# Kernel optimization log

Measured on AMD Instinct MI355X. Metric: run time of the kernel, lower is better.

## Reference

```python
import jax, jax.numpy as jnp
import numpy as np


def setup_inputs() -> dict:
    key = jax.random.key(0)
    B, T, UNITS = 8, 4096, 1024
    # per-timestep features: [x, y, z_0..z_{units-1}]
    inputs = jax.random.normal(key, (B, T, UNITS + 2), dtype=jnp.float32)
    return {"inputs": inputs}


def reference(inputs) -> jnp.ndarray:
    # Faithful translation of CLSProcess wrapped in an RNN over time
    # (return_sequences): state_t = y_t * state_{t-1} + x_t * z_t, state_0 = 0.
    B, T, F = inputs.shape
    units = F - 2
    x = inputs[..., 0:1]   # [B,T,1]  input gate
    y = inputs[..., 1:2]   # [B,T,1]  decay gate
    z = inputs[..., 2:]    # [B,T,units]
    xz = x * z             # [B,T,units] precompute elementwise product

    y_t = jnp.moveaxis(y, 1, 0)    # [T,B,1]
    xz_t = jnp.moveaxis(xz, 1, 0)  # [T,B,units]

    def step(prev, yt_xzt):
        yt, xzt = yt_xzt
        out = yt * prev + xzt      # diagonal linear recurrence
        return out, out

    init = jnp.zeros((B, units), dtype=inputs.dtype)
    _, outs = jax.lax.scan(step, init, (y_t, xz_t))  # outs: [T,B,units]
    return jnp.moveaxis(outs, 0, 1)                  # [B,T,units]
```

## Files before the change

### kernel.cpp

```cpp
#include <hip/hip_runtime.h>


#define BB 8
#define TT 4096
#define FF 1026
#define UU 1024
#define CC 128
#define NC 32

typedef float f2 __attribute__((ext_vector_type(2)));


__global__ __launch_bounds__(256) void k_partial(const float* __restrict__ in,
                                                 float* __restrict__ A,
                                                 float* __restrict__ Bc) {
    int bid   = blockIdx.x;
    int s     = bid & 1;
    int chunk = (bid >> 1) & (NC - 1);
    int b     = bid >> 6;
    int u     = s * 512 + threadIdx.x * 2;

    const float* row = in + ((size_t)b * TT + (size_t)chunk * CC) * FF;
    float accx = 0.f, accy = 0.f, yprod = 1.f;
#pragma unroll 8
    for (int t = 0; t < CC; ++t) {
        f2 xy = *reinterpret_cast<const f2*>(row + (size_t)t * FF);
        f2 z  = *reinterpret_cast<const f2*>(row + (size_t)t * FF + 2 + u);
        accx  = fmaf(xy.y, accx, xy.x * z.x);
        accy  = fmaf(xy.y, accy, xy.x * z.y);
        yprod *= xy.y;
    }
    f2 o; o.x = accx; o.y = accy;
    *reinterpret_cast<f2*>(Bc + ((size_t)b * NC + chunk) * UU + u) = o;
    if (threadIdx.x == 0 && s == 0) A[b * NC + chunk] = yprod;
}

__global__ __launch_bounds__(256) void k_scan(const float* __restrict__ A,
                                              float* __restrict__ Bc) {
    int tid = blockIdx.x * 256 + threadIdx.x;
    int b   = tid / (UU / 2);
    int u   = (tid % (UU / 2)) * 2;
    float cx = 0.f, cy = 0.f;
#pragma unroll
    for (int c = 0; c < NC; ++c) {
        float a = A[b * NC + c];
        f2* p = reinterpret_cast<f2*>(Bc + ((size_t)b * NC + c) * UU + u);
        f2 bv = *p;
        cx = fmaf(a, cx, bv.x);
        cy = fmaf(a, cy, bv.y);
        f2 o; o.x = cx; o.y = cy;
        *p = o;
    }
}

__global__ __launch_bounds__(256) void k_final(const float* __restrict__ in,
                                               const float* __restrict__ Bc,
                                               float* __restrict__ out) {
    int bid   = blockIdx.x;
    int s     = bid & 1;
    int chunk = (bid >> 1) & (NC - 1);
    int b     = bid >> 6;
    int u     = s * 512 + threadIdx.x * 2;

    const float* row  = in  + ((size_t)b * TT + (size_t)chunk * CC) * FF;
    float*       orow = out + ((size_t)b * TT + (size_t)chunk * CC) * UU + u;

    float accx = 0.f, accy = 0.f;
    if (chunk != 0) {
        f2 cv = *reinterpret_cast<const f2*>(
            Bc + ((size_t)b * NC + (chunk - 1)) * UU + u);
        accx = cv.x; accy = cv.y;
    }
#pragma unroll 8
    for (int t = 0; t < CC; ++t) {
        f2 xy = *reinterpret_cast<const f2*>(row + (size_t)t * FF);
        f2 z  = *reinterpret_cast<const f2*>(row + (size_t)t * FF + 2 + u);
        accx = fmaf(xy.y, accx, xy.x * z.x);
        accy = fmaf(xy.y, accy, xy.x * z.y);
        f2 o; o.x = accx; o.y = accy;
        __builtin_nontemporal_store(o, reinterpret_cast<f2*>(orow + (size_t)t * UU));
    }
}

extern "C" void kernel_launch(void* const* d_in, const int* in_sizes, int n_in,
                              void* d_out, int out_size, void* d_ws, size_t ws_size,
                              hipStream_t stream) {
    const float* in  = (const float*)d_in[0];
    float*       out = (float*)d_out;
    float*       A   = (float*)d_ws;
    float*       Bc  = A + BB * NC;

    k_partial<<<BB * NC * 2, 256, 0, stream>>>(in, A, Bc);
    k_scan<<<(BB * UU / 2) / 256, 256, 0, stream>>>(A, Bc);
    k_final<<<BB * NC * 2, 256, 0, stream>>>(in, Bc, out);
}
```

Measured before the change: 70.52 us.

## Fuse carry scan into final kernel and double chunk count

Removes the separate k_scan launch. Each k_final block now recomputes its incoming carry by serially combining all earlier chunk partials from the workspace. The chunk count rises from 32 to 64 when the workspace is large enough, which halves the serial time loop per block and doubles the grid. In exchange, later chunks read up to 63 extra partial vectors each, adding redundant L2 traffic, and this path depends on the available workspace size.

```diff
diff --git a/kernel.cpp b/kernel.cpp
--- a/kernel.cpp
+++ b/kernel.cpp
@@ -5,19 +5,19 @@
 #define TT 4096
 #define FF 1026
 #define UU 1024
-#define CC 128
-#define NC 32
 
 typedef float f2 __attribute__((ext_vector_type(2)));
 
-
+template <int NC>
 __global__ __launch_bounds__(256) void k_partial(const float* __restrict__ in,
                                                  float* __restrict__ A,
                                                  float* __restrict__ Bc) {
+    constexpr int CC = TT / NC;
+    constexpr int LOG2NC = (NC == 64) ? 6 : 5;
     int bid   = blockIdx.x;
     int s     = bid & 1;
     int chunk = (bid >> 1) & (NC - 1);
-    int b     = bid >> 6;
+    int b     = bid >> (1 + LOG2NC);
     int u     = s * 512 + threadIdx.x * 2;
 
     const float* row = in + ((size_t)b * TT + (size_t)chunk * CC) * FF;
@@ -35,42 +35,34 @@
     if (threadIdx.x == 0 && s == 0) A[b * NC + chunk] = yprod;
 }
 
-__global__ __launch_bounds__(256) void k_scan(const float* __restrict__ A,
-                                              float* __restrict__ Bc) {
-    int tid = blockIdx.x * 256 + threadIdx.x;
-    int b   = tid / (UU / 2);
-    int u   = (tid % (UU / 2)) * 2;
-    float cx = 0.f, cy = 0.f;
-#pragma unroll
-    for (int c = 0; c < NC; ++c) {
-        float a = A[b * NC + c];
-        f2* p = reinterpret_cast<f2*>(Bc + ((size_t)b * NC + c) * UU + u);
-        f2 bv = *p;
-        cx = fmaf(a, cx, bv.x);
-        cy = fmaf(a, cy, bv.y);
-        f2 o; o.x = cx; o.y = cy;
-        *p = o;
-    }
-}
-
+template <int NC>
 __global__ __launch_bounds__(256) void k_final(const float* __restrict__ in,
+                                               const float* __restrict__ A,
                                                const float* __restrict__ Bc,
                                                float* __restrict__ out) {
+    constexpr int CC = TT / NC;
+    constexpr int LOG2NC = (NC == 64) ? 6 : 5;
     int bid   = blockIdx.x;
     int s     = bid & 1;
     int chunk = (bid >> 1) & (NC - 1);
-    int b     = bid >> 6;
+    int b     = bid >> (1 + LOG2NC);
     int u     = s * 512 + threadIdx.x * 2;
+
+    float accx = 0.f, accy = 0.f;
+    {
+        const float* Ab = A + b * NC;
+        const float* Bb = Bc + (size_t)b * NC * UU + u;
+        for (int c = 0; c < chunk; ++c) {
+            float a = Ab[c];
+            f2 bv = *reinterpret_cast<const f2*>(Bb + (size_t)c * UU);
+            accx = fmaf(a, accx, bv.x);
+            accy = fmaf(a, accy, bv.y);
+        }
+    }
 
     const float* row  = in  + ((size_t)b * TT + (size_t)chunk * CC) * FF;
     float*       orow = out + ((size_t)b * TT + (size_t)chunk * CC) * UU + u;
 
-    float accx = 0.f, accy = 0.f;
-    if (chunk != 0) {
-        f2 cv = *reinterpret_cast<const f2*>(
-            Bc + ((size_t)b * NC + (chunk - 1)) * UU + u);
-        accx = cv.x; accy = cv.y;
-    }
 #pragma unroll 8
     for (int t = 0; t < CC; ++t) {
         f2 xy = *reinterpret_cast<const f2*>(row + (size_t)t * FF);
@@ -88,9 +80,17 @@
     const float* in  = (const float*)d_in[0];
     float*       out = (float*)d_out;
     float*       A   = (float*)d_ws;
-    float*       Bc  = A + BB * NC;
 
-    k_partial<<<BB * NC * 2, 256, 0, stream>>>(in, A, Bc);
-    k_scan<<<(BB * UU / 2) / 256, 256, 0, stream>>>(A, Bc);
-    k_final<<<BB * NC * 2, 256, 0, stream>>>(in, Bc, out);
+    const size_t need64 = (size_t)(BB * 64 + BB * 64 * UU) * sizeof(float);
+    if (ws_size >= need64) {
+        constexpr int NC = 64;
+        float* Bc = A + BB * NC;
+        k_partial<NC><<<BB * NC * 2, 256, 0, stream>>>(in, A, Bc);
+        k_final<NC><<<BB * NC * 2, 256, 0, stream>>>(in, A, Bc, out);
+    } else {
+        constexpr int NC = 32;
+        float* Bc = A + BB * NC;
+        k_partial<NC><<<BB * NC * 2, 256, 0, stream>>>(in, A, Bc);
+        k_final<NC><<<BB * NC * 2, 256, 0, stream>>>(in, A, Bc, out);
+    }
 }
```

Result: slower. 73.51 us (+4.2%).
